# Kernel optimization log

Hardware: AMD Instinct MI355X
Metric: run time of the kernel (lower is better)

Reference implementation:

```python
import jax, jax.numpy as jnp
import numpy as np

B, C, T = 4, 512, 2048
H = 8
GROUPS = 32


def setup_inputs() -> dict:
    key = jax.random.key(0)
    ks = jax.random.split(key, 7)
    x = jax.random.normal(ks[0], (B, C, T), dtype=jnp.float32)
    norm_w = jnp.ones((C,), dtype=jnp.float32)
    norm_b = jnp.zeros((C,), dtype=jnp.float32)
    # conv1d kernel-size-1 weights -> plain [out, in] matrices
    qkv_w = jax.random.normal(ks[1], (3 * C, C), dtype=jnp.float32) / np.sqrt(C)
    qkv_b = jnp.zeros((3 * C,), dtype=jnp.float32)
    proj_w = jax.random.normal(ks[2], (C, C), dtype=jnp.float32) / np.sqrt(C)
    proj_b = jnp.zeros((C,), dtype=jnp.float32)
    return {"x": x, "norm_w": norm_w, "norm_b": norm_b,
            "qkv_w": qkv_w, "qkv_b": qkv_b,
            "proj_w": proj_w, "proj_b": proj_b}


def _group_norm(x, w, b, groups=GROUPS, eps=1e-5):
    # x: [B, C, T]
    b_, c_, t_ = x.shape
    xg = x.reshape(b_, groups, c_ // groups, t_)
    mean = jnp.mean(xg, axis=(2, 3), keepdims=True)
    var = jnp.var(xg, axis=(2, 3), keepdims=True)
    xg = (xg - mean) * jax.lax.rsqrt(var + eps)
    xn = xg.reshape(b_, c_, t_)
    return xn * w[None, :, None] + b[None, :, None]


def reference(x, norm_w, norm_b, qkv_w, qkv_b, proj_w, proj_b):
    b, c, t = x.shape
    ch = c // H  # per-head channels
    scale = 1.0 / np.sqrt(np.sqrt(ch))

    xn = _group_norm(x, norm_w, norm_b)
    # 1x1 conv over T: [B, 3C, T]
    qkv = jnp.einsum('oc,bct->bot', qkv_w, xn) + qkv_b[None, :, None]
    q, k, v = jnp.split(qkv, 3, axis=1)               # each [B, C, T]
    q = q.reshape(b * H, ch, t)
    k = k.reshape(b * H, ch, t)
    v = v.reshape(b * H, ch, t)

    # full attention scores [B*H, T, T]
    weight = jnp.einsum('bct,bcs->bts', q * scale, k * scale)
    weight = jax.nn.softmax(weight.astype(jnp.float32), axis=-1).astype(weight.dtype)
    a = jnp.einsum('bts,bcs->bct', weight, v)          # [B*H, ch, T]
    h = a.reshape(b, c, t)

    h = jnp.einsum('oc,bct->bot', proj_w, h) + proj_b[None, :, None]
    return x + h
```

## Files before the change

kernel.cpp:

```cpp
#include <hip/hip_runtime.h>

#define NB 4
#define NC 512
#define NT 2048
#define NH 8
#define CHD 64
#define NG 32
#define GC 16
#define QK_SCALE 0.35355339059327373f
#define LOG2E 1.4426950408889634f

typedef __bf16 bf16_t;
typedef __bf16 bf16x8 __attribute__((ext_vector_type(8)));
typedef __bf16 bf16x4 __attribute__((ext_vector_type(4)));
typedef __bf16 bf16x2 __attribute__((ext_vector_type(2)));
typedef float f32x4 __attribute__((ext_vector_type(4)));
typedef float f32x16 __attribute__((ext_vector_type(16)));
typedef int i32x2 __attribute__((ext_vector_type(2)));
typedef unsigned int u32;

#if __has_builtin(__builtin_amdgcn_exp2f)
#define EXP2F(x) __builtin_amdgcn_exp2f(x)
#else
#define EXP2F(x) __exp2f(x)
#endif

__device__ __forceinline__ int probe_isbf(const void* norm_w) {
  return *(const unsigned*)norm_w == 0x3F803F80u;
}

__device__ __forceinline__ float load_sc(const void* p, int isbf, int i) {
  return isbf ? (float)((const bf16_t*)p)[i] : ((const float*)p)[i];
}

__device__ __forceinline__ u32 pk2bf(float a, float b) {
  union { bf16x2 h; u32 u; } c;
  c.h[0] = (bf16_t)a; c.h[1] = (bf16_t)b;
  return c.u;
}

__global__ __launch_bounds__(256) void sma_cvt_w(
    const void* __restrict__ Wqkv, const void* __restrict__ Wproj,
    const void* __restrict__ probe, bf16_t* __restrict__ wqb,
    bf16_t* __restrict__ wpb) {
  const int isbf = probe_isbf(probe);
  const size_t NQ = (size_t)3 * NC * NC;
  const size_t e = ((size_t)blockIdx.x * 256 + threadIdx.x) * 8;
  const void* src;
  bf16_t* dst;
  size_t off;
  if (e < NQ) { src = Wqkv; dst = wqb; off = e; }
  else        { src = Wproj; dst = wpb; off = e - NQ; }
  if (isbf) {
    *(bf16x8*)&dst[off] = *(const bf16x8*)&((const bf16_t*)src)[off];
  } else {
    const float* s = (const float*)src + off;
    const float4 a = *(const float4*)s;
    const float4 b2 = *(const float4*)(s + 4);
    bf16x8 o;
    o[0] = (bf16_t)a.x;  o[1] = (bf16_t)a.y;  o[2] = (bf16_t)a.z;  o[3] = (bf16_t)a.w;
    o[4] = (bf16_t)b2.x; o[5] = (bf16_t)b2.y; o[6] = (bf16_t)b2.z; o[7] = (bf16_t)b2.w;
    *(bf16x8*)&dst[off] = o;
  }
}

__global__ __launch_bounds__(256) void sma_gn_stats(
    const void* __restrict__ xv, const void* __restrict__ probe,
    float* __restrict__ partial) {
  const int isbf = probe_isbf(probe);
  const int blk = blockIdx.x;
  const size_t base = (size_t)blk * 8 * NT;

  float s = 0.f, ss = 0.f;
  if (isbf) {
    const bf16_t* xp = (const bf16_t*)xv + base;
    for (int i = threadIdx.x; i < 2048; i += 256) {
      bf16x8 v = *(const bf16x8*)&xp[(size_t)i * 8];
#pragma unroll
      for (int j = 0; j < 8; ++j) { float f = (float)v[j]; s += f; ss += f * f; }
    }
  } else {
    const float* xp = (const float*)xv + base;
    for (int i = threadIdx.x; i < 4096; i += 256) {
      float4 v = *(const float4*)&xp[(size_t)i * 4];
      s += v.x + v.y + v.z + v.w;
      ss += v.x * v.x + v.y * v.y + v.z * v.z + v.w * v.w;
    }
  }
#pragma unroll
  for (int m = 32; m; m >>= 1) { s += __shfl_xor(s, m); ss += __shfl_xor(ss, m); }
  __shared__ float red[2][4];
  const int wave = threadIdx.x >> 6, lane = threadIdx.x & 63;
  if (lane == 0) { red[0][wave] = s; red[1][wave] = ss; }
  __syncthreads();
  if (threadIdx.x == 0) {
    partial[blk * 2] = red[0][0] + red[0][1] + red[0][2] + red[0][3];
    partial[blk * 2 + 1] = red[1][0] + red[1][1] + red[1][2] + red[1][3];
  }
}

__global__ __launch_bounds__(256) void sma_gn_apply(
    const void* __restrict__ xv, const void* __restrict__ wv,
    const void* __restrict__ bv, const float* __restrict__ partial,
    bf16_t* __restrict__ xnT) {
  const int isbf = probe_isbf(wv);
  const int bb = blockIdx.x >> 6;
  const int tc = blockIdx.x & 63;
  const int t0 = tc * 32;
  const int tid = threadIdx.x;

  __shared__ float gs[NG][2];
  __shared__ float scsb[NC][2];
  __shared__ bf16_t XT[32][520];

  if (tid < NG) {
    const int p0 = (bb * 64 + tid * 2) * 2;
    const float s = partial[p0] + partial[p0 + 2];
    const float ss = partial[p0 + 1] + partial[p0 + 3];
    const float mean = s * (1.f / 32768.f);
    const float var = ss * (1.f / 32768.f) - mean * mean;
    gs[tid][0] = mean;
    gs[tid][1] = rsqrtf(var + 1e-5f);
  }
  __syncthreads();
  for (int c = tid; c < NC; c += 256) {
    const int g = c >> 4;
    const float sc = load_sc(wv, isbf, c) * gs[g][1];
    scsb[c][0] = sc;
    scsb[c][1] = load_sc(bv, isbf, c) - gs[g][0] * sc;
  }
  __syncthreads();

  if (isbf) {
    const bf16_t* xp = (const bf16_t*)xv + (size_t)bb * NC * NT;
#pragma unroll
    for (int i = 0; i < 8; ++i) {
      const int idx = tid + i * 256;
      const int c = idx >> 2, tv = idx & 3;
      bf16x8 v = *(const bf16x8*)&xp[(size_t)c * NT + t0 + tv * 8];
      const float sc = scsb[c][0], sb = scsb[c][1];
#pragma unroll
      for (int j = 0; j < 8; ++j) XT[tv * 8 + j][c] = (bf16_t)((float)v[j] * sc + sb);
    }
  } else {
    const float* xp = (const float*)xv + (size_t)bb * NC * NT;
#pragma unroll
    for (int i = 0; i < 16; ++i) {
      const int idx = tid + i * 256;
      const int c = idx >> 3, tv = idx & 7;
      float4 v = *(const float4*)&xp[(size_t)c * NT + t0 + tv * 4];
      const float sc = scsb[c][0], sb = scsb[c][1];
      XT[tv * 4 + 0][c] = (bf16_t)(v.x * sc + sb);
      XT[tv * 4 + 1][c] = (bf16_t)(v.y * sc + sb);
      XT[tv * 4 + 2][c] = (bf16_t)(v.z * sc + sb);
      XT[tv * 4 + 3][c] = (bf16_t)(v.w * sc + sb);
    }
  }
  __syncthreads();
  bf16_t* op = xnT + ((size_t)bb * NT + t0) * NC;
#pragma unroll
  for (int i = 0; i < 8; ++i) {
    const int idx = tid + i * 256;
    const int t = idx >> 6, cl = idx & 63;
    *(bf16x8*)&op[(size_t)t * NC + cl * 8] = *(const bf16x8*)&XT[t][cl * 8];
  }
}

__global__ __launch_bounds__(256) void sma_qkv_kernel(
    const bf16_t* __restrict__ W, const void* __restrict__ biasv,
    const void* __restrict__ probe, const bf16_t* __restrict__ xnT,
    bf16_t* __restrict__ qT, bf16_t* __restrict__ kT, bf16_t* __restrict__ vO) {
  const int isbf = probe_isbf(probe);
  const int nb = blockIdx.x;
  const int mb = blockIdx.y;
  const int tid = threadIdx.x;
  const int lane = tid & 63, wave = tid >> 6;
  const int l15 = lane & 15, quad = lane >> 4;
  const int wm = wave >> 1, wn = wave & 1;

  __shared__ bf16_t As[128][72];
  __shared__ bf16_t Bs[128][72];

  const int m0 = mb * 128, n0 = nb * 128;

  f32x4 acc[4][4];
#pragma unroll
  for (int i = 0; i < 4; ++i)
#pragma unroll
    for (int j = 0; j < 4; ++j) acc[i][j] = (f32x4){0.f, 0.f, 0.f, 0.f};

  bf16x8 ar[4], br[4];
#pragma unroll
  for (int it = 0; it < 4; ++it) {
    const int idx = tid + it * 256;
    const int row = idx >> 3, cv = idx & 7;
    ar[it] = *(const bf16x8*)&W[(size_t)(m0 + row) * NC + cv * 8];
    br[it] = *(const bf16x8*)&xnT[(size_t)(n0 + row) * NC + cv * 8];
  }

  for (int k0 = 0; k0 < NC; k0 += 64) {
    if (k0) __syncthreads();
#pragma unroll
    for (int it = 0; it < 4; ++it) {
      const int idx = tid + it * 256;
      const int row = idx >> 3, cv = idx & 7;
      *(bf16x8*)&As[row][cv * 8] = ar[it];
      *(bf16x8*)&Bs[row][cv * 8] = br[it];
    }
    __syncthreads();
    if (k0 + 64 < NC) {
      const int k1 = k0 + 64;
#pragma unroll
      for (int it = 0; it < 4; ++it) {
        const int idx = tid + it * 256;
        const int row = idx >> 3, cv = idx & 7;
        ar[it] = *(const bf16x8*)&W[(size_t)(m0 + row) * NC + k1 + cv * 8];
        br[it] = *(const bf16x8*)&xnT[(size_t)(n0 + row) * NC + k1 + cv * 8];
      }
    }
#pragma unroll
    for (int ks = 0; ks < 2; ++ks) {
      bf16x8 af[4], bfr[4];
#pragma unroll
      for (int mi = 0; mi < 4; ++mi)
        af[mi] = *(const bf16x8*)&As[wm * 64 + mi * 16 + l15][ks * 32 + quad * 8];
#pragma unroll
      for (int ni = 0; ni < 4; ++ni)
        bfr[ni] = *(const bf16x8*)&Bs[wn * 64 + ni * 16 + l15][ks * 32 + quad * 8];
#pragma unroll
      for (int mi = 0; mi < 4; ++mi)
#pragma unroll
        for (int ni = 0; ni < 4; ++ni)
          acc[mi][ni] = __builtin_amdgcn_mfma_f32_16x16x32_bf16(
              af[mi], bfr[ni], acc[mi][ni], 0, 0, 0);
    }
  }

  const int mw0 = m0 + wm * 64;
  const int bb = n0 >> 11;
  const int tbase = (n0 & 2047) + wn * 64;
  if (mw0 < 2 * NC) {
    bf16_t* dst = (mw0 < NC) ? qT : kT;
    const float scale = (mw0 < NC) ? (QK_SCALE * LOG2E) : QK_SCALE;
    const int h = (mw0 & (NC - 1)) >> 6;
#pragma unroll
    for (int mi = 0; mi < 4; ++mi) {
      const int ch0 = mi * 16 + quad * 4;
      float bs[4];
#pragma unroll
      for (int r = 0; r < 4; ++r) bs[r] = load_sc(biasv, isbf, mw0 + ch0 + r);
#pragma unroll
      for (int ni = 0; ni < 4; ++ni) {
        const int t = tbase + ni * 16 + l15;
        bf16x4 pk;
#pragma unroll
        for (int r = 0; r < 4; ++r)
          pk[r] = (bf16_t)((acc[mi][ni][r] + bs[r]) * scale);
        *(bf16x4*)&dst[((size_t)(bb * NH + h) * NT + t) * CHD + ch0] = pk;
      }
    }
  } else {
#pragma unroll
    for (int mi = 0; mi < 4; ++mi) {
#pragma unroll
      for (int r = 0; r < 4; ++r) {
        const int og = mw0 + mi * 16 + quad * 4 + r;
        const float bsc = load_sc(biasv, isbf, og);
        const int oc = og - 2 * NC;
#pragma unroll
        for (int ni = 0; ni < 4; ++ni) {
          const int t = tbase + ni * 16 + l15;
          vO[((size_t)bb * NC + oc) * NT + t] = (bf16_t)(acc[mi][ni][r] + bsc);
        }
      }
    }
  }
}

__global__ __launch_bounds__(512) void sma_attn_kernel(
    const bf16_t* __restrict__ qT, const bf16_t* __restrict__ kT,
    const bf16_t* __restrict__ vO, bf16_t* __restrict__ ht) {
  const int id = blockIdx.x;
  const int bh = id & 31, qt = id >> 5;
  const int b = bh >> 3, h = bh & 7;
  const int tid = threadIdx.x;
  const int lane = tid & 63, wave = tid >> 6;
  const int l31 = lane & 31, half = lane >> 5;

  const bf16_t* qb = qT + (size_t)bh * NT * CHD;
  const bf16_t* kb = kT + (size_t)bh * NT * CHD;
  const bf16_t* vb = vO + ((size_t)b * NC + h * CHD) * NT;

  __shared__ bf16_t Ks[64 * 64];
  __shared__ bf16_t Vs[64 * 64];
  __shared__ float lS[8][32];

  const int tq = qt * 256 + wave * 32 + l31;
  bf16x8 qf[4];
#pragma unroll
  for (int kc = 0; kc < 4; ++kc)
    qf[kc] = *(const bf16x8*)&qb[(size_t)tq * CHD + kc * 16 + half * 8];

  const int sR = tid >> 3;
  const int cvC = tid & 7;
  bf16x8 kr, vr;
  kr = *(const bf16x8*)&kb[(size_t)sR * CHD + cvC * 8];
  vr = *(const bf16x8*)&vb[(size_t)sR * NT + cvC * 8];

  f32x16 Oa[2];
#pragma unroll
  for (int i = 0; i < 2; ++i)
#pragma unroll
    for (int r = 0; r < 16; ++r) Oa[i][r] = 0.f;
  float lacc = 0.f;

  for (int st = 0; st < NT / 64; ++st) {
    __syncthreads();
    *(bf16x8*)&Ks[sR * 64 + ((cvC ^ (sR & 7)) * 8)] = kr;
    *(bf16x8*)&Vs[sR * 64 + ((cvC ^ (sR & 7)) * 8)] = vr;
    __syncthreads();
    if (st < NT / 64 - 1) {
      const int s0 = (st + 1) * 64;
      kr = *(const bf16x8*)&kb[(size_t)(s0 + sR) * CHD + cvC * 8];
      vr = *(const bf16x8*)&vb[(size_t)sR * NT + s0 + cvC * 8];
    }

    f32x16 sa[2];
#pragma unroll
    for (int i = 0; i < 2; ++i)
#pragma unroll
      for (int r = 0; r < 16; ++r) sa[i][r] = 0.f;
#pragma unroll
    for (int kc = 0; kc < 4; ++kc) {
#pragma unroll
      for (int sub = 0; sub < 2; ++sub) {
        const int srow = sub * 32 + l31;
        bf16x8 kf = *(const bf16x8*)&Ks[srow * 64 + (((kc * 2 + half) ^ (srow & 7)) * 8)];
        sa[sub] = __builtin_amdgcn_mfma_f32_32x32x16_bf16(kf, qf[kc], sa[sub], 0, 0, 0);
      }
    }

#pragma unroll
    for (int sub = 0; sub < 2; ++sub)
#pragma unroll
      for (int r = 0; r < 16; ++r) {
        const float p = EXP2F(sa[sub][r]);
        sa[sub][r] = p;
        lacc += p;
      }

    bf16x8 pfrag[4];
#pragma unroll
    for (int sub = 0; sub < 2; ++sub) {
#pragma unroll
      for (int kk = 0; kk < 2; ++kk) {
        const int b0 = kk * 8;
        const u32 E0 = pk2bf(sa[sub][b0 + 0], sa[sub][b0 + 1]);
        const u32 E1 = pk2bf(sa[sub][b0 + 2], sa[sub][b0 + 3]);
        const u32 O0 = pk2bf(sa[sub][b0 + 4], sa[sub][b0 + 5]);
        const u32 O1 = pk2bf(sa[sub][b0 + 6], sa[sub][b0 + 7]);
        const i32x2 sw0 = __builtin_amdgcn_permlane32_swap((int)E0, (int)O0, false, false);
        const i32x2 sw1 = __builtin_amdgcn_permlane32_swap((int)E1, (int)O1, false, false);
        union { u32 w[4]; bf16x8 v; } f;
        f.w[0] = (u32)sw0[0]; f.w[1] = (u32)sw1[0];
        f.w[2] = (u32)sw0[1]; f.w[3] = (u32)sw1[1];
        pfrag[sub * 2 + kk] = f.v;
      }
    }

#pragma unroll
    for (int ksp = 0; ksp < 4; ++ksp) {
#pragma unroll
      for (int sub = 0; sub < 2; ++sub) {
        const int crow = sub * 32 + l31;
        bf16x8 vf = *(const bf16x8*)&Vs[crow * 64 + (((ksp * 2 + half) ^ (crow & 7)) * 8)];
        Oa[sub] = __builtin_amdgcn_mfma_f32_32x32x16_bf16(pfrag[ksp], vf, Oa[sub], 0, 0, 0);
      }
    }
  }

  const float ltot = lacc + __shfl_xor(lacc, 32);
  if (half == 0) lS[wave][l31] = ltot;
  float invr[16];
#pragma unroll
  for (int rg = 0; rg < 4; ++rg) {
    const float4 l4 = *(const float4*)&lS[wave][rg * 8 + half * 4];
    invr[rg * 4 + 0] = 1.f / l4.x; invr[rg * 4 + 1] = 1.f / l4.y;
    invr[rg * 4 + 2] = 1.f / l4.z; invr[rg * 4 + 3] = 1.f / l4.w;
  }
#pragma unroll
  for (int sub = 0; sub < 2; ++sub) {
    const int c = h * CHD + sub * 32 + l31;
#pragma unroll
    for (int reg = 0; reg < 16; ++reg) {
      const int trow = (reg & 3) + 8 * (reg >> 2) + 4 * half;
      const int t = qt * 256 + wave * 32 + trow;
      ht[((size_t)b * NT + t) * NC + c] = (bf16_t)(Oa[sub][reg] * invr[reg]);
    }
  }
}

__global__ __launch_bounds__(256) void sma_proj_kernel(
    const bf16_t* __restrict__ W, const void* __restrict__ biasv,
    const void* __restrict__ probe, const bf16_t* __restrict__ ht,
    const void* __restrict__ xv, void* __restrict__ outv) {
  const int isbf = probe_isbf(probe);
  const int nb = blockIdx.x;
  const int mb = blockIdx.y;
  const int tid = threadIdx.x;
  const int lane = tid & 63, wave = tid >> 6;
  const int l15 = lane & 15, quad = lane >> 4;
  const int wm = wave >> 1, wn = wave & 1;

  __shared__ bf16_t As[64][72];
  __shared__ bf16_t Bs[128][72];

  const int m0 = mb * 64, n0 = nb * 128;

  f32x4 acc[2][4];
#pragma unroll
  for (int i = 0; i < 2; ++i)
#pragma unroll
    for (int j = 0; j < 4; ++j) acc[i][j] = (f32x4){0.f, 0.f, 0.f, 0.f};

  bf16x8 ar[2], br[4];
#pragma unroll
  for (int it = 0; it < 2; ++it) {
    const int idx = tid + it * 256;
    const int row = idx >> 3, cv = idx & 7;
    ar[it] = *(const bf16x8*)&W[(size_t)(m0 + row) * NC + cv * 8];
  }
#pragma unroll
  for (int it = 0; it < 4; ++it) {
    const int idx = tid + it * 256;
    const int row = idx >> 3, cv = idx & 7;
    br[it] = *(const bf16x8*)&ht[(size_t)(n0 + row) * NC + cv * 8];
  }

  for (int k0 = 0; k0 < NC; k0 += 64) {
    if (k0) __syncthreads();
#pragma unroll
    for (int it = 0; it < 2; ++it) {
      const int idx = tid + it * 256;
      const int row = idx >> 3, cv = idx & 7;
      *(bf16x8*)&As[row][cv * 8] = ar[it];
    }
#pragma unroll
    for (int it = 0; it < 4; ++it) {
      const int idx = tid + it * 256;
      const int row = idx >> 3, cv = idx & 7;
      *(bf16x8*)&Bs[row][cv * 8] = br[it];
    }
    __syncthreads();
    if (k0 + 64 < NC) {
      const int k1 = k0 + 64;
#pragma unroll
      for (int it = 0; it < 2; ++it) {
        const int idx = tid + it * 256;
        const int row = idx >> 3, cv = idx & 7;
        ar[it] = *(const bf16x8*)&W[(size_t)(m0 + row) * NC + k1 + cv * 8];
      }
#pragma unroll
      for (int it = 0; it < 4; ++it) {
        const int idx = tid + it * 256;
        const int row = idx >> 3, cv = idx & 7;
        br[it] = *(const bf16x8*)&ht[(size_t)(n0 + row) * NC + k1 + cv * 8];
      }
    }
#pragma unroll
    for (int ks = 0; ks < 2; ++ks) {
      bf16x8 af[2], bfr[4];
#pragma unroll
      for (int mi = 0; mi < 2; ++mi)
        af[mi] = *(const bf16x8*)&As[wm * 32 + mi * 16 + l15][ks * 32 + quad * 8];
#pragma unroll
      for (int ni = 0; ni < 4; ++ni)
        bfr[ni] = *(const bf16x8*)&Bs[wn * 64 + ni * 16 + l15][ks * 32 + quad * 8];
#pragma unroll
      for (int mi = 0; mi < 2; ++mi)
#pragma unroll
        for (int ni = 0; ni < 4; ++ni)
          acc[mi][ni] = __builtin_amdgcn_mfma_f32_16x16x32_bf16(
              af[mi], bfr[ni], acc[mi][ni], 0, 0, 0);
    }
  }

  const int bb = n0 >> 11;
  const int tbase = (n0 & 2047) + wn * 64;
  if (isbf) {
    const bf16_t* xb = (const bf16_t*)xv;
    bf16_t* op = (bf16_t*)outv;
#pragma unroll
    for (int mi = 0; mi < 2; ++mi)
#pragma unroll
      for (int r = 0; r < 4; ++r) {
        const int o = m0 + wm * 32 + mi * 16 + quad * 4 + r;
        const float bsc = load_sc(biasv, 1, o);
#pragma unroll
        for (int ni = 0; ni < 4; ++ni) {
          const int t = tbase + ni * 16 + l15;
          const size_t oi = ((size_t)bb * NC + o) * NT + t;
          op[oi] = (bf16_t)(acc[mi][ni][r] + bsc + (float)xb[oi]);
        }
      }
  } else {
    const float* xb = (const float*)xv;
    float* op = (float*)outv;
#pragma unroll
    for (int mi = 0; mi < 2; ++mi)
#pragma unroll
      for (int r = 0; r < 4; ++r) {
        const int o = m0 + wm * 32 + mi * 16 + quad * 4 + r;
        const float bsc = load_sc(biasv, 0, o);
#pragma unroll
        for (int ni = 0; ni < 4; ++ni) {
          const int t = tbase + ni * 16 + l15;
          const size_t oi = ((size_t)bb * NC + o) * NT + t;
          op[oi] = acc[mi][ni][r] + bsc + xb[oi];
        }
      }
  }
}

extern "C" void kernel_launch(void* const* d_in, const int* in_sizes, int n_in,
                              void* d_out, int out_size, void* d_ws, size_t ws_size,
                              hipStream_t stream) {
  const size_t NE = (size_t)NB * NC * NT;
  float* partial = (float*)d_ws;
  bf16_t* xnT = (bf16_t*)((char*)d_ws + 4096);
  bf16_t* qTp = xnT + NE;
  bf16_t* kTp = qTp + NE;
  bf16_t* vOp = kTp + NE;
  bf16_t* htp = vOp + NE;
  bf16_t* wqb = htp + NE;
  bf16_t* wpb = wqb + (size_t)3 * NC * NC;

  sma_cvt_w<<<dim3(512), 256, 0, stream>>>(d_in[3], d_in[5], d_in[1], wqb, wpb);
  sma_gn_stats<<<dim3(256), 256, 0, stream>>>(d_in[0], d_in[1], partial);
  sma_gn_apply<<<dim3(256), 256, 0, stream>>>(d_in[0], d_in[1], d_in[2], partial, xnT);
  sma_qkv_kernel<<<dim3(64, 12), 256, 0, stream>>>(
      wqb, d_in[4], d_in[1], xnT, qTp, kTp, vOp);
  sma_attn_kernel<<<dim3(256), 512, 0, stream>>>(qTp, kTp, vOp, htp);
  sma_proj_kernel<<<dim3(64, 8), 256, 0, stream>>>(
      wpb, d_in[6], d_in[1], htp, d_in[0], d_out);
}
```

Before: 163.1 us.

## Load K/V fragments directly from global into registers, drop LDS staging

The attention kernel no longer stages K and V tiles through shared memory with two barriers per step. Each wave now loads its MFMA operand fragments for K and V straight from global memory into registers, prefetches the next K tile, and raises wave priority around the MFMA blocks. This removes the LDS traffic and block-wide syncs, but each of the 8 waves now fetches the same K/V data independently from global or L2. It also raises register pressure and leaves little latency hiding for the V loads.

Measured after the change: 240.9 us. 47.7% more time.

```diff
diff --git a/kernel.cpp b/kernel.cpp
--- a/kernel.cpp
+++ b/kernel.cpp
@@ -291,8 +291,6 @@
   const bf16_t* kb = kT + (size_t)bh * NT * CHD;
   const bf16_t* vb = vO + ((size_t)b * NC + h * CHD) * NT;
 
-  __shared__ bf16_t Ks[64 * 64];
-  __shared__ bf16_t Vs[64 * 64];
   __shared__ float lS[8][32];
 
   const int tq = qt * 256 + wave * 32 + l31;
@@ -301,43 +299,58 @@
   for (int kc = 0; kc < 4; ++kc)
     qf[kc] = *(const bf16x8*)&qb[(size_t)tq * CHD + kc * 16 + half * 8];
 
-  const int sR = tid >> 3;
-  const int cvC = tid & 7;
-  bf16x8 kr, vr;
-  kr = *(const bf16x8*)&kb[(size_t)sR * CHD + cvC * 8];
-  vr = *(const bf16x8*)&vb[(size_t)sR * NT + cvC * 8];
+  const bf16_t* kb0 = kb + (size_t)l31 * CHD + half * 8;
+  const bf16_t* vb0 = vb + (size_t)l31 * NT + half * 8;
 
   f32x16 Oa[2];
 #pragma unroll
   for (int i = 0; i < 2; ++i)
 #pragma unroll
     for (int r = 0; r < 16; ++r) Oa[i][r] = 0.f;
+  f32x16 z16;
+#pragma unroll
+  for (int r = 0; r < 16; ++r) z16[r] = 0.f;
   float lacc = 0.f;
 
-  for (int st = 0; st < NT / 64; ++st) {
-    __syncthreads();
-    *(bf16x8*)&Ks[sR * 64 + ((cvC ^ (sR & 7)) * 8)] = kr;
-    *(bf16x8*)&Vs[sR * 64 + ((cvC ^ (sR & 7)) * 8)] = vr;
-    __syncthreads();
-    if (st < NT / 64 - 1) {
-      const int s0 = (st + 1) * 64;
-      kr = *(const bf16x8*)&kb[(size_t)(s0 + sR) * CHD + cvC * 8];
-      vr = *(const bf16x8*)&vb[(size_t)sR * NT + s0 + cvC * 8];
-    }
-
+  bf16x8 kf[8];
+#pragma unroll
+  for (int kc = 0; kc < 4; ++kc)
+#pragma unroll
+    for (int sub = 0; sub < 2; ++sub)
+      kf[kc * 2 + sub] = *(const bf16x8*)&kb0[(size_t)sub * 32 * CHD + kc * 16];
+
+  const int NS = NT / 64;
+#pragma unroll 2
+  for (int st = 0; st < NS; ++st) {
     f32x16 sa[2];
-#pragma unroll
-    for (int i = 0; i < 2; ++i)
-#pragma unroll
-      for (int r = 0; r < 16; ++r) sa[i][r] = 0.f;
-#pragma unroll
-    for (int kc = 0; kc < 4; ++kc) {
-#pragma unroll
-      for (int sub = 0; sub < 2; ++sub) {
-        const int srow = sub * 32 + l31;
-        bf16x8 kf = *(const bf16x8*)&Ks[srow * 64 + (((kc * 2 + half) ^ (srow & 7)) * 8)];
-        sa[sub] = __builtin_amdgcn_mfma_f32_32x32x16_bf16(kf, qf[kc], sa[sub], 0, 0, 0);
-      }
+    __builtin_amdgcn_s_setprio(1);
+#pragma unroll
+    for (int sub = 0; sub < 2; ++sub)
+      sa[sub] = __builtin_amdgcn_mfma_f32_32x32x16_bf16(kf[sub], qf[0], z16, 0, 0, 0);
+#pragma unroll
+    for (int kc = 1; kc < 4; ++kc)
+#pragma unroll
+      for (int sub = 0; sub < 2; ++sub)
+        sa[sub] = __builtin_amdgcn_mfma_f32_32x32x16_bf16(
+            kf[kc * 2 + sub], qf[kc], sa[sub], 0, 0, 0);
+    __builtin_amdgcn_s_setprio(0);
+
+    bf16x8 vf[8];
+    {
+      const bf16_t* vt = vb0 + st * 64;
+#pragma unroll
+      for (int ksp = 0; ksp < 4; ++ksp)
+#pragma unroll
+        for (int sub = 0; sub < 2; ++sub)
+          vf[ksp * 2 + sub] = *(const bf16x8*)&vt[(size_t)sub * 32 * NT + ksp * 16];
+    }
+    if (st < NS - 1) {
+      const bf16_t* kt = kb0 + (size_t)(st + 1) * 64 * CHD;
+#pragma unroll
+      for (int kc = 0; kc < 4; ++kc)
+#pragma unroll
+        for (int sub = 0; sub < 2; ++sub)
+          kf[kc * 2 + sub] = *(const bf16x8*)&kt[(size_t)sub * 32 * CHD + kc * 16];
     }
 
 #pragma unroll
@@ -368,15 +381,14 @@
       }
     }
 
-#pragma unroll
-    for (int ksp = 0; ksp < 4; ++ksp) {
-#pragma unroll
-      for (int sub = 0; sub < 2; ++sub) {
-        const int crow = sub * 32 + l31;
-        bf16x8 vf = *(const bf16x8*)&Vs[crow * 64 + (((ksp * 2 + half) ^ (crow & 7)) * 8)];
-        Oa[sub] = __builtin_amdgcn_mfma_f32_32x32x16_bf16(pfrag[ksp], vf, Oa[sub], 0, 0, 0);
-      }
-    }
+    __builtin_amdgcn_s_setprio(1);
+#pragma unroll
+    for (int ksp = 0; ksp < 4; ++ksp)
+#pragma unroll
+      for (int sub = 0; sub < 2; ++sub)
+        Oa[sub] = __builtin_amdgcn_mfma_f32_32x32x16_bf16(
+            pfrag[ksp], vf[ksp * 2 + sub], Oa[sub], 0, 0, 0);
+    __builtin_amdgcn_s_setprio(0);
   }
 
   const float ltot = lacc + __shfl_xor(lacc, 32);
```

## Double-buffer 128-wide K/V tiles in padded LDS with a single barrier per step

Applied to the files above, without the earlier changes.

The attention kernel now stages 128 key/value positions per iteration instead of 64. It alternates between two LDS buffers, so each step needs only one __syncthreads instead of two. The XOR swizzle is replaced by row padding (66 and 130 element strides), and the first QK MFMA of each step starts from a zero vector rather than a zeroed accumulator. This halves loop iterations and barriers and gives more work per step, at the cost of roughly 67KB of LDS per block. The padded strides are not 16-byte aligned, which may force 128-bit LDS accesses to be split into narrower ones.

Result: slower. 251.2 us (+54.1%).

```diff
diff --git a/kernel.cpp b/kernel.cpp
--- a/kernel.cpp
+++ b/kernel.cpp
@@ -277,6 +277,8 @@
   }
 }
 
+#define KLDP 66
+#define VLDP 130
 __global__ __launch_bounds__(512) void sma_attn_kernel(
     const bf16_t* __restrict__ qT, const bf16_t* __restrict__ kT,
     const bf16_t* __restrict__ vO, bf16_t* __restrict__ ht) {
@@ -291,8 +293,8 @@
   const bf16_t* kb = kT + (size_t)bh * NT * CHD;
   const bf16_t* vb = vO + ((size_t)b * NC + h * CHD) * NT;
 
-  __shared__ bf16_t Ks[64 * 64];
-  __shared__ bf16_t Vs[64 * 64];
+  __shared__ bf16_t Ks[2][128 * KLDP];
+  __shared__ bf16_t Vs[2][64 * VLDP];
   __shared__ float lS[8][32];
 
   const int tq = qt * 256 + wave * 32 + l31;
@@ -303,55 +305,65 @@
 
   const int sR = tid >> 3;
   const int cvC = tid & 7;
-  bf16x8 kr, vr;
-  kr = *(const bf16x8*)&kb[(size_t)sR * CHD + cvC * 8];
-  vr = *(const bf16x8*)&vb[(size_t)sR * NT + cvC * 8];
+  const int vR = tid >> 4;
+  const int cV = tid & 15;
+  bf16x8 kr0, kr1, vr0, vr1;
+  kr0 = *(const bf16x8*)&kb[(size_t)sR * CHD + cvC * 8];
+  kr1 = *(const bf16x8*)&kb[(size_t)(sR + 64) * CHD + cvC * 8];
+  vr0 = *(const bf16x8*)&vb[(size_t)vR * NT + cV * 8];
+  vr1 = *(const bf16x8*)&vb[(size_t)(vR + 32) * NT + cV * 8];
 
   f32x16 Oa[2];
 #pragma unroll
   for (int i = 0; i < 2; ++i)
 #pragma unroll
     for (int r = 0; r < 16; ++r) Oa[i][r] = 0.f;
+  f32x16 z16;
+#pragma unroll
+  for (int r = 0; r < 16; ++r) z16[r] = 0.f;
   float lacc = 0.f;
 
-  for (int st = 0; st < NT / 64; ++st) {
+  const int NS = NT / 128;
+  for (int st = 0; st < NS; ++st) {
+    bf16_t* Kb = Ks[st & 1];
+    bf16_t* Vb = Vs[st & 1];
+    *(bf16x8*)&Kb[sR * KLDP + cvC * 8] = kr0;
+    *(bf16x8*)&Kb[(sR + 64) * KLDP + cvC * 8] = kr1;
+    *(bf16x8*)&Vb[vR * VLDP + cV * 8] = vr0;
+    *(bf16x8*)&Vb[(vR + 32) * VLDP + cV * 8] = vr1;
     __syncthreads();
-    *(bf16x8*)&Ks[sR * 64 + ((cvC ^ (sR & 7)) * 8)] = kr;
-    *(bf16x8*)&Vs[sR * 64 + ((cvC ^ (sR & 7)) * 8)] = vr;
-    __syncthreads();
-    if (st < NT / 64 - 1) {
-      const int s0 = (st + 1) * 64;
-      kr = *(const bf16x8*)&kb[(size_t)(s0 + sR) * CHD + cvC * 8];
-      vr = *(const bf16x8*)&vb[(size_t)sR * NT + s0 + cvC * 8];
-    }
-
-    f32x16 sa[2];
-#pragma unroll
-    for (int i = 0; i < 2; ++i)
-#pragma unroll
-      for (int r = 0; r < 16; ++r) sa[i][r] = 0.f;
-#pragma unroll
-    for (int kc = 0; kc < 4; ++kc) {
-#pragma unroll
-      for (int sub = 0; sub < 2; ++sub) {
-        const int srow = sub * 32 + l31;
-        bf16x8 kf = *(const bf16x8*)&Ks[srow * 64 + (((kc * 2 + half) ^ (srow & 7)) * 8)];
+    if (st < NS - 1) {
+      const int s0 = (st + 1) * 128;
+      kr0 = *(const bf16x8*)&kb[(size_t)(s0 + sR) * CHD + cvC * 8];
+      kr1 = *(const bf16x8*)&kb[(size_t)(s0 + sR + 64) * CHD + cvC * 8];
+      vr0 = *(const bf16x8*)&vb[(size_t)vR * NT + s0 + cV * 8];
+      vr1 = *(const bf16x8*)&vb[(size_t)(vR + 32) * NT + s0 + cV * 8];
+    }
+
+    f32x16 sa[4];
+#pragma unroll
+    for (int sub = 0; sub < 4; ++sub) {
+      const int srow = sub * 32 + l31;
+      {
+        bf16x8 kf = *(const bf16x8*)&Kb[srow * KLDP + half * 8];
+        sa[sub] = __builtin_amdgcn_mfma_f32_32x32x16_bf16(kf, qf[0], z16, 0, 0, 0);
+      }
+#pragma unroll
+      for (int kc = 1; kc < 4; ++kc) {
+        bf16x8 kf = *(const bf16x8*)&Kb[srow * KLDP + (kc * 2 + half) * 8];
         sa[sub] = __builtin_amdgcn_mfma_f32_32x32x16_bf16(kf, qf[kc], sa[sub], 0, 0, 0);
       }
     }
 
-#pragma unroll
-    for (int sub = 0; sub < 2; ++sub)
+    bf16x8 pfrag[8];
+#pragma unroll
+    for (int sub = 0; sub < 4; ++sub) {
 #pragma unroll
       for (int r = 0; r < 16; ++r) {
         const float p = EXP2F(sa[sub][r]);
         sa[sub][r] = p;
         lacc += p;
       }
-
-    bf16x8 pfrag[4];
-#pragma unroll
-    for (int sub = 0; sub < 2; ++sub) {
 #pragma unroll
       for (int kk = 0; kk < 2; ++kk) {
         const int b0 = kk * 8;
@@ -369,12 +381,12 @@
     }
 
 #pragma unroll
-    for (int ksp = 0; ksp < 4; ++ksp) {
-#pragma unroll
-      for (int sub = 0; sub < 2; ++sub) {
-        const int crow = sub * 32 + l31;
-        bf16x8 vf = *(const bf16x8*)&Vs[crow * 64 + (((ksp * 2 + half) ^ (crow & 7)) * 8)];
-        Oa[sub] = __builtin_amdgcn_mfma_f32_32x32x16_bf16(pfrag[ksp], vf, Oa[sub], 0, 0, 0);
+    for (int ksp = 0; ksp < 8; ++ksp) {
+#pragma unroll
+      for (int subc = 0; subc < 2; ++subc) {
+        const int crow = subc * 32 + l31;
+        bf16x8 vf = *(const bf16x8*)&Vb[crow * VLDP + (ksp * 2 + half) * 8];
+        Oa[subc] = __builtin_amdgcn_mfma_f32_32x32x16_bf16(pfrag[ksp], vf, Oa[subc], 0, 0, 0);
       }
     }
   }
```

## Use direct global-to-LDS loads with XOR swizzle in GEMMs and attention

Applied to the files above, without the earlier changes.

Replaces the register-staged global loads plus LDS stores in the QKV GEMM, projection GEMM and attention kernel with global_load_lds direct-to-LDS transfers. Padded LDS tiles become XOR-swizzled unpadded layouts. Attention gains a double-buffered K/V tile so the next tile's load is issued before compute on the current one, saving a barrier per step. The GEMMs lose their register prefetch of the next k-slice, so they now rely on the async LDS path and wave overlap, which may expose load latency. The change relies on barriers alone to order the async loads, with no explicit vmcnt wait.

Measured after the change: 173.2 us. 6.2% more time.

```diff
diff --git a/kernel.cpp b/kernel.cpp
--- a/kernel.cpp
+++ b/kernel.cpp
@@ -24,6 +24,12 @@
 #else
 #define EXP2F(x) __exp2f(x)
 #endif
+
+__device__ __forceinline__ void gload_lds16(const bf16_t* g, bf16_t* l) {
+  __builtin_amdgcn_global_load_lds(
+      (const __attribute__((address_space(1))) void*)g,
+      (__attribute__((address_space(3))) void*)l, 16, 0, 0);
+}
 
 __device__ __forceinline__ int probe_isbf(const void* norm_w) {
   return *(const unsigned*)norm_w == 0x3F803F80u;
@@ -178,8 +184,8 @@
   const int l15 = lane & 15, quad = lane >> 4;
   const int wm = wave >> 1, wn = wave & 1;
 
-  __shared__ bf16_t As[128][72];
-  __shared__ bf16_t Bs[128][72];
+  __shared__ bf16_t As[128 * 64];
+  __shared__ bf16_t Bs[128 * 64];
 
   const int m0 = mb * 128, n0 = nb * 128;
 
@@ -189,44 +195,32 @@
 #pragma unroll
     for (int j = 0; j < 4; ++j) acc[i][j] = (f32x4){0.f, 0.f, 0.f, 0.f};
 
-  bf16x8 ar[4], br[4];
-#pragma unroll
-  for (int it = 0; it < 4; ++it) {
-    const int idx = tid + it * 256;
-    const int row = idx >> 3, cv = idx & 7;
-    ar[it] = *(const bf16x8*)&W[(size_t)(m0 + row) * NC + cv * 8];
-    br[it] = *(const bf16x8*)&xnT[(size_t)(n0 + row) * NC + cv * 8];
-  }
+  const int rA = lane >> 3;
+  const int chk = lane & 7;
+  const int schk = (chk ^ rA) * 8;
 
   for (int k0 = 0; k0 < NC; k0 += 64) {
-    if (k0) __syncthreads();
 #pragma unroll
     for (int it = 0; it < 4; ++it) {
-      const int idx = tid + it * 256;
-      const int row = idx >> 3, cv = idx & 7;
-      *(bf16x8*)&As[row][cv * 8] = ar[it];
-      *(bf16x8*)&Bs[row][cv * 8] = br[it];
+      const int rb = (it * 4 + wave) * 8;
+      const int row = rb + rA;
+      gload_lds16(&W[(size_t)(m0 + row) * NC + k0 + schk], &As[rb * 64]);
+      gload_lds16(&xnT[(size_t)(n0 + row) * NC + k0 + schk], &Bs[rb * 64]);
     }
     __syncthreads();
-    if (k0 + 64 < NC) {
-      const int k1 = k0 + 64;
-#pragma unroll
-      for (int it = 0; it < 4; ++it) {
-        const int idx = tid + it * 256;
-        const int row = idx >> 3, cv = idx & 7;
-        ar[it] = *(const bf16x8*)&W[(size_t)(m0 + row) * NC + k1 + cv * 8];
-        br[it] = *(const bf16x8*)&xnT[(size_t)(n0 + row) * NC + k1 + cv * 8];
-      }
-    }
 #pragma unroll
     for (int ks = 0; ks < 2; ++ks) {
       bf16x8 af[4], bfr[4];
 #pragma unroll
-      for (int mi = 0; mi < 4; ++mi)
-        af[mi] = *(const bf16x8*)&As[wm * 64 + mi * 16 + l15][ks * 32 + quad * 8];
-#pragma unroll
-      for (int ni = 0; ni < 4; ++ni)
-        bfr[ni] = *(const bf16x8*)&Bs[wn * 64 + ni * 16 + l15][ks * 32 + quad * 8];
+      for (int mi = 0; mi < 4; ++mi) {
+        const int row = wm * 64 + mi * 16 + l15;
+        af[mi] = *(const bf16x8*)&As[row * 64 + (((ks * 4 + quad) ^ (row & 7)) * 8)];
+      }
+#pragma unroll
+      for (int ni = 0; ni < 4; ++ni) {
+        const int row = wn * 64 + ni * 16 + l15;
+        bfr[ni] = *(const bf16x8*)&Bs[row * 64 + (((ks * 4 + quad) ^ (row & 7)) * 8)];
+      }
 #pragma unroll
       for (int mi = 0; mi < 4; ++mi)
 #pragma unroll
@@ -234,6 +228,7 @@
           acc[mi][ni] = __builtin_amdgcn_mfma_f32_16x16x32_bf16(
               af[mi], bfr[ni], acc[mi][ni], 0, 0, 0);
     }
+    __syncthreads();
   }
 
   const int mw0 = m0 + wm * 64;
@@ -291,8 +286,8 @@
   const bf16_t* kb = kT + (size_t)bh * NT * CHD;
   const bf16_t* vb = vO + ((size_t)b * NC + h * CHD) * NT;
 
-  __shared__ bf16_t Ks[64 * 64];
-  __shared__ bf16_t Vs[64 * 64];
+  __shared__ bf16_t Ks[2][64 * 64];
+  __shared__ bf16_t Vs[2][64 * 64];
   __shared__ float lS[8][32];
 
   const int tq = qt * 256 + wave * 32 + l31;
@@ -301,41 +296,53 @@
   for (int kc = 0; kc < 4; ++kc)
     qf[kc] = *(const bf16x8*)&qb[(size_t)tq * CHD + kc * 16 + half * 8];
 
-  const int sR = tid >> 3;
-  const int cvC = tid & 7;
-  bf16x8 kr, vr;
-  kr = *(const bf16x8*)&kb[(size_t)sR * CHD + cvC * 8];
-  vr = *(const bf16x8*)&vb[(size_t)sR * NT + cvC * 8];
+  const int sRw = wave * 8 + (lane >> 3);
+  const int chk = lane & 7;
+  const int schk = (chk ^ (sRw & 7)) * 8;
+  const bf16_t* ksrc = kb + (size_t)sRw * CHD + schk;
+  const bf16_t* vsrc = vb + (size_t)sRw * NT + schk;
+  bf16_t* kdstw0 = &Ks[0][wave * 8 * 64];
+  bf16_t* kdstw1 = &Ks[1][wave * 8 * 64];
+  bf16_t* vdstw0 = &Vs[0][wave * 8 * 64];
+  bf16_t* vdstw1 = &Vs[1][wave * 8 * 64];
+
+  gload_lds16(ksrc, kdstw0);
+  gload_lds16(vsrc, vdstw0);
 
   f32x16 Oa[2];
 #pragma unroll
   for (int i = 0; i < 2; ++i)
 #pragma unroll
     for (int r = 0; r < 16; ++r) Oa[i][r] = 0.f;
+  f32x16 z16;
+#pragma unroll
+  for (int r = 0; r < 16; ++r) z16[r] = 0.f;
   float lacc = 0.f;
 
-  for (int st = 0; st < NT / 64; ++st) {
+  const int NS = NT / 64;
+  for (int st = 0; st < NS; ++st) {
     __syncthreads();
-    *(bf16x8*)&Ks[sR * 64 + ((cvC ^ (sR & 7)) * 8)] = kr;
-    *(bf16x8*)&Vs[sR * 64 + ((cvC ^ (sR & 7)) * 8)] = vr;
-    __syncthreads();
-    if (st < NT / 64 - 1) {
+    if (st + 1 < NS) {
       const int s0 = (st + 1) * 64;
-      kr = *(const bf16x8*)&kb[(size_t)(s0 + sR) * CHD + cvC * 8];
-      vr = *(const bf16x8*)&vb[(size_t)sR * NT + s0 + cvC * 8];
-    }
+      gload_lds16(ksrc + (size_t)s0 * CHD, ((st + 1) & 1) ? kdstw1 : kdstw0);
+      gload_lds16(vsrc + s0,               ((st + 1) & 1) ? vdstw1 : vdstw0);
+    }
+    const bf16_t* Kb = Ks[st & 1];
+    const bf16_t* Vb = Vs[st & 1];
 
     f32x16 sa[2];
 #pragma unroll
-    for (int i = 0; i < 2; ++i)
-#pragma unroll
-      for (int r = 0; r < 16; ++r) sa[i][r] = 0.f;
-#pragma unroll
-    for (int kc = 0; kc < 4; ++kc) {
+    for (int sub = 0; sub < 2; ++sub) {
+      const int srow = sub * 32 + l31;
+      bf16x8 kf = *(const bf16x8*)&Kb[srow * 64 + ((half ^ (srow & 7)) * 8)];
+      sa[sub] = __builtin_amdgcn_mfma_f32_32x32x16_bf16(kf, qf[0], z16, 0, 0, 0);
+    }
+#pragma unroll
+    for (int kc = 1; kc < 4; ++kc) {
 #pragma unroll
       for (int sub = 0; sub < 2; ++sub) {
         const int srow = sub * 32 + l31;
-        bf16x8 kf = *(const bf16x8*)&Ks[srow * 64 + (((kc * 2 + half) ^ (srow & 7)) * 8)];
+        bf16x8 kf = *(const bf16x8*)&Kb[srow * 64 + (((kc * 2 + half) ^ (srow & 7)) * 8)];
         sa[sub] = __builtin_amdgcn_mfma_f32_32x32x16_bf16(kf, qf[kc], sa[sub], 0, 0, 0);
       }
     }
@@ -373,7 +380,7 @@
 #pragma unroll
       for (int sub = 0; sub < 2; ++sub) {
         const int crow = sub * 32 + l31;
-        bf16x8 vf = *(const bf16x8*)&Vs[crow * 64 + (((ksp * 2 + half) ^ (crow & 7)) * 8)];
+        bf16x8 vf = *(const bf16x8*)&Vb[crow * 64 + (((ksp * 2 + half) ^ (crow & 7)) * 8)];
         Oa[sub] = __builtin_amdgcn_mfma_f32_32x32x16_bf16(pfrag[ksp], vf, Oa[sub], 0, 0, 0);
       }
     }
@@ -412,8 +419,8 @@
   const int l15 = lane & 15, quad = lane >> 4;
   const int wm = wave >> 1, wn = wave & 1;
 
-  __shared__ bf16_t As[64][72];
-  __shared__ bf16_t Bs[128][72];
+  __shared__ bf16_t As[64 * 64];
+  __shared__ bf16_t Bs[128 * 64];
 
   const int m0 = mb * 64, n0 = nb * 128;
 
@@ -423,59 +430,37 @@
 #pragma unroll
     for (int j = 0; j < 4; ++j) acc[i][j] = (f32x4){0.f, 0.f, 0.f, 0.f};
 
-  bf16x8 ar[2], br[4];
-#pragma unroll
-  for (int it = 0; it < 2; ++it) {
-    const int idx = tid + it * 256;
-    const int row = idx >> 3, cv = idx & 7;
-    ar[it] = *(const bf16x8*)&W[(size_t)(m0 + row) * NC + cv * 8];
-  }
-#pragma unroll
-  for (int it = 0; it < 4; ++it) {
-    const int idx = tid + it * 256;
-    const int row = idx >> 3, cv = idx & 7;
-    br[it] = *(const bf16x8*)&ht[(size_t)(n0 + row) * NC + cv * 8];
-  }
+  const int rA = lane >> 3;
+  const int chk = lane & 7;
+  const int schk = (chk ^ rA) * 8;
 
   for (int k0 = 0; k0 < NC; k0 += 64) {
-    if (k0) __syncthreads();
 #pragma unroll
     for (int it = 0; it < 2; ++it) {
-      const int idx = tid + it * 256;
-      const int row = idx >> 3, cv = idx & 7;
-      *(bf16x8*)&As[row][cv * 8] = ar[it];
+      const int rb = (it * 4 + wave) * 8;
+      const int row = rb + rA;
+      gload_lds16(&W[(size_t)(m0 + row) * NC + k0 + schk], &As[rb * 64]);
     }
 #pragma unroll
     for (int it = 0; it < 4; ++it) {
-      const int idx = tid + it * 256;
-      const int row = idx >> 3, cv = idx & 7;
-      *(bf16x8*)&Bs[row][cv * 8] = br[it];
+      const int rb = (it * 4 + wave) * 8;
+      const int row = rb + rA;
+      gload_lds16(&ht[(size_t)(n0 + row) * NC + k0 + schk], &Bs[rb * 64]);
     }
     __syncthreads();
-    if (k0 + 64 < NC) {
-      const int k1 = k0 + 64;
-#pragma unroll
-      for (int it = 0; it < 2; ++it) {
-        const int idx = tid + it * 256;
-        const int row = idx >> 3, cv = idx & 7;
-        ar[it] = *(const bf16x8*)&W[(size_t)(m0 + row) * NC + k1 + cv * 8];
-      }
-#pragma unroll
-      for (int it = 0; it < 4; ++it) {
-        const int idx = tid + it * 256;
-        const int row = idx >> 3, cv = idx & 7;
-        br[it] = *(const bf16x8*)&ht[(size_t)(n0 + row) * NC + k1 + cv * 8];
-      }
-    }
 #pragma unroll
     for (int ks = 0; ks < 2; ++ks) {
       bf16x8 af[2], bfr[4];
 #pragma unroll
-      for (int mi = 0; mi < 2; ++mi)
-        af[mi] = *(const bf16x8*)&As[wm * 32 + mi * 16 + l15][ks * 32 + quad * 8];
-#pragma unroll
-      for (int ni = 0; ni < 4; ++ni)
-        bfr[ni] = *(const bf16x8*)&Bs[wn * 64 + ni * 16 + l15][ks * 32 + quad * 8];
+      for (int mi = 0; mi < 2; ++mi) {
+        const int row = wm * 32 + mi * 16 + l15;
+        af[mi] = *(const bf16x8*)&As[row * 64 + (((ks * 4 + quad) ^ (row & 7)) * 8)];
+      }
+#pragma unroll
+      for (int ni = 0; ni < 4; ++ni) {
+        const int row = wn * 64 + ni * 16 + l15;
+        bfr[ni] = *(const bf16x8*)&Bs[row * 64 + (((ks * 4 + quad) ^ (row & 7)) * 8)];
+      }
 #pragma unroll
       for (int mi = 0; mi < 2; ++mi)
 #pragma unroll
@@ -483,6 +468,7 @@
           acc[mi][ni] = __builtin_amdgcn_mfma_f32_16x16x32_bf16(
               af[mi], bfr[ni], acc[mi][ni], 0, 0, 0);
     }
+    __syncthreads();
   }
 
   const int bb = n0 >> 11;
```
